# Kernel tuning notes

Measured on AMD Instinct MI355X. Metric: run time of the kernel, lower is better.

## Reference

```python
import jax, jax.numpy as jnp
import numpy as np

STEP, LEAK = 16, 32
KS = STEP + LEAK          # kernel_size = 48
FODEP = KS                # forced depression window
SYNAPSES, NEURONS = 64, 256
IC, OC = 1, 10
DENSE = 0.5
THETA = DENSE * SYNAPSES * IC   # 32.0
BIAS = 0.5
BATCH, TIME = 16, 512


def setup_inputs() -> dict:
    key = jax.random.key(0)
    k1, k2 = jax.random.split(key)
    # binary input spikes, density 0.2
    input_spikes = (jax.random.uniform(k1, (BATCH, IC, SYNAPSES, TIME)) < 0.2).astype(jnp.float32)
    # weight ~ Exponential(rate=1/w_init=2).sample().clip(0,1), mean 0.5
    u = jax.random.uniform(k2, (OC * NEURONS, IC * SYNAPSES), minval=1e-6, maxval=1.0)
    weight = jnp.clip(-0.5 * jnp.log(u), 0.0, 1.0)
    return {"input_spikes": input_spikes, "weight": weight}


def _step_fire_leak_kernel(weight):
    # kernel[o, i, t] = max(0, min(t/step, -(t - w*step)/leak + w)), flipped on t
    t = jnp.arange(KS, dtype=weight.dtype)
    t_spike = t / STEP                                        # rising edge
    t_leak = -(t - weight[..., None] * STEP) / LEAK + weight[..., None]  # decaying edge
    kernel = jnp.maximum(jnp.zeros((), weight.dtype), jnp.minimum(t_spike, t_leak))
    return kernel[..., ::-1]


def _forward(input_spikes, weight):
    B, C, S, T = input_spikes.shape
    x = input_spikes.reshape(B, C * S, T)
    kernel = _step_fire_leak_kernel(weight)                   # [OC*N, IC*S, KS]
    # conv1d with padding = kernel_size on both sides -> T' = T + KS + 1
    pot = jax.lax.conv_general_dilated(
        x, kernel, window_strides=(1,), padding=[(KS, KS)],
        dimension_numbers=("NCH", "OIH", "NCH"))
    Tp = pot.shape[-1]
    pot = pot.reshape(B, OC, NEURONS, Tp) + BIAS * THETA      # unsupervised bias path

    # winner-takes-all scan over time with per-(batch, neuron) depression counter
    pot_t = pot.transpose(3, 0, 2, 1)                         # [T', B, N, OC]
    dep0 = jnp.zeros((B, NEURONS, OC), jnp.int32)

    def step_fn(dep, p):
        masked = jnp.where(dep == 0, p, jnp.zeros((), p.dtype))
        winner = jnp.argmax(masked, axis=-1)                  # [B, N]
        wpot = jnp.take_along_axis(masked, winner[..., None], axis=-1)[..., 0]
        spike = (wpot > THETA).astype(p.dtype)                # [B, N]
        w_t = jax.nn.one_hot(winner, OC, dtype=p.dtype) * spike[..., None]
        dep = jnp.clip(dep + spike.astype(jnp.int32)[..., None] * FODEP - 1, 0, FODEP - 1)
        return dep, w_t

    _, winners = jax.lax.scan(step_fn, dep0, pot_t)           # [T', B, N, OC]
    return winners.transpose(1, 3, 2, 0)                      # [B, OC, N, T'] float


def reference(input_spikes, weight):
    return _forward(input_spikes, weight)
```

## Files before the change

kernel.cpp:

```cpp
#include <hip/hip_runtime.h>

#define B_   16
#define OC_  10
#define N_   256
#define O_   2560
#define S_   64
#define T_   512
#define KS_  48
#define TP_  561
#define TT   24
#define WROW 72

#define NOC   160
#define XROWS 624
#define JC    6
#define NPH   (KS_/JC)

#define SCH    16
#define CPITCH 572

using i32x4 = __attribute__((ext_vector_type(4))) int;

__global__ void prep_all(const float* __restrict__ x, const float* __restrict__ w,
                         unsigned char* __restrict__ xb, signed char* __restrict__ Bg) {
    if (blockIdx.x < 2048) {
        int idx = blockIdx.x * 256 + threadIdx.x;
        int t = idx & 511;
        int bi = idx >> 9;
        int i = bi & 63, b = bi >> 6;
        xb[((size_t)(b * 512 + t) << 6) + i] = (x[idx] != 0.0f) ? 1 : 0;
    } else {
        int idx = (blockIdx.x - 2048) * 256 + threadIdx.x;
        int i = idx & 63;
        int oj = idx >> 6;
        int j = oj % KS_, o = oj / KS_;
        float wv = w[(o << 6) + i];
        float rise = (float)j * 0.0625f;
        float leak = -((float)j - wv * 16.0f) * 0.03125f + wv;
        float kv   = fmaxf(0.0f, fminf(rise, leak));
        int q  = (int)lrintf(kv * 4194304.0f);
        int d0 = ((q + 128) & 255) - 128;
        int q1 = (q - d0) >> 8;
        int d1 = ((q1 + 128) & 255) - 128;
        int d2 = (q1 - d1) >> 8;
        int oc = o >> 4, ol = o & 15;
        int jm = j & 15, jh = j >> 4;
        int pos = jm * 3 + jh;
        int key = (ol >> 1) & 3;
        int bpos = ((((i >> 4) ^ key) << 4) | (i & 15));
        size_t base = (((size_t)(oc * KS_ + pos) * 48) + ol) * 64 + bpos;
        Bg[base]            = (signed char)d0;
        Bg[base + 16 * 64]  = (signed char)d1;
        Bg[base + 32 * 64]  = (signed char)d2;
    }
}

__global__ __launch_bounds__(256, 2) void gemm_i8(
    const unsigned char* __restrict__ xb,
    const signed char*  __restrict__ Bg,
    float* __restrict__ pot)
{
    __shared__ __align__(16) unsigned char xT[XROWS * 64];
    __shared__ __align__(16) signed char  Bst[2][JC * 48 * 64];

    const int tid  = threadIdx.x;
    const int lane = tid & 63;
    const int wave = tid >> 6;
    const int oc = blockIdx.x;
    const int b  = blockIdx.y;
    const int lrow = lane & 15;
    const int quad = lane >> 4;
    const int tw = wave * 144;
    const int coffB = ((quad ^ ((lrow >> 1) & 3)) << 4);

    const signed char* BgBase = Bg + (size_t)oc * KS_ * 48 * 64;

    auto stage = [&](int ph, int buf) {
        const signed char* src = BgBase + (size_t)(ph * JC) * 48 * 64;
        signed char* dst = &Bst[buf][0];
        for (int c = tid; c < JC * 48 * 64 / 16; c += 256)
            __builtin_amdgcn_global_load_lds(
                (const __attribute__((address_space(1))) void*)(src + c * 16),
                (__attribute__((address_space(3))) void*)(dst + c * 16),
                16, 0, 0);
    };

    stage(0, 0);

    for (int z = tid; z < 112 * 4; z += 256) {
        int zi = z >> 2, p = z & 3;
        int r = (zi < 49) ? zi : (561 + zi - 49);
        *(i32x4*)(xT + r * 64 + p * 16) = (i32x4){0, 0, 0, 0};
    }
    const unsigned char* xbb = xb + ((size_t)b << 15);
    for (int q = tid; q < 2048; q += 256) {
        i32x4 v = *(const i32x4*)(xbb + q * 16);
        int t = q >> 2, p = q & 3;
        int r = 49 + t;
        *(i32x4*)(xT + r * 64 + ((p ^ ((r >> 1) & 3)) << 4)) = v;
    }

    i32x4 acc[9][3];
#pragma unroll
    for (int mi = 0; mi < 9; ++mi)
#pragma unroll
        for (int f = 0; f < 3; ++f)
            acc[mi][f] = (i32x4){0, 0, 0, 0};

    __syncthreads();

    for (int ph = 0; ph < NPH; ++ph) {
        if (ph + 1 < NPH) stage(ph + 1, (ph + 1) & 1);
        const signed char* cb = &Bst[ph & 1][0];
#pragma unroll
        for (int tloc = 0; tloc < 2; ++tloc) {
            const int j0 = ph * 2 + tloc;
            const int rb = tw + 16 - j0 + lrow;
            const int coffA = ((quad ^ ((rb >> 1) & 3)) << 4);
            i32x4 af[11], bf[3][3];
#pragma unroll
            for (int k = 0; k < 11; ++k)
                af[k] = *(const i32x4*)(xT + (rb + k * 16) * 64 + coffA);
#pragma unroll
            for (int jh = 0; jh < 3; ++jh)
#pragma unroll
                for (int f = 0; f < 3; ++f)
                    bf[jh][f] = *(const i32x4*)
                        (cb + (((tloc * 3 + jh) * 48) + f * 16 + lrow) * 64 + coffB);
            __builtin_amdgcn_s_setprio(1);
#pragma unroll
            for (int jh = 0; jh < 3; ++jh)
#pragma unroll
                for (int mi = 0; mi < 9; ++mi)
#pragma unroll
                    for (int f = 0; f < 3; ++f)
                        acc[mi][f] = __builtin_amdgcn_mfma_i32_16x16x64_i8(
                            af[mi + 2 - jh], bf[jh][f], acc[mi][f], 0, 0, 0);
            __builtin_amdgcn_s_setprio(0);
        }
        __syncthreads();
    }

    const size_t potb = (size_t)b * TP_;
#pragma unroll
    for (int mi = 0; mi < 9; ++mi) {
#pragma unroll
        for (int r = 0; r < 4; ++r) {
            int t = tw + mi * 16 + quad * 4 + r;
            if (t < TP_) {
                double pq = ((double)acc[mi][0][r]
                           + 256.0   * (double)acc[mi][1][r]
                           + 65536.0 * (double)acc[mi][2][r])
                          * (1.0 / 4194304.0);
                pot[(potb + t) * O_ + oc * 16 + lrow] = (float)pq;
            }
        }
    }
}

__global__ __launch_bounds__(1024) void scan_fused(
    const float* __restrict__ pot,
    float* __restrict__ out)
{
    __shared__ unsigned char codeW[SCH * CPITCH];
    __shared__ unsigned char ocW[SCH * CPITCH];

    const int tid = threadIdx.x;
    const int nc = blockIdx.x;
    const int b  = blockIdx.y;
    const int n0 = nc * SCH;

    for (int pair = tid; pair < TP_ * SCH; pair += 1024) {
        int t = pair >> 4, nl = pair & 15;
        const float* p = pot + ((size_t)(b * TP_ + t)) * O_ + n0 + nl;
        float best = p[0]; int bo = 0;
#pragma unroll
        for (int ch = 1; ch < OC_; ++ch) {
            float v = p[ch * N_];
            if (v > best) { best = v; bo = ch; }
        }
        codeW[nl * CPITCH + t] =
            ((best + 16.0f) > 32.0f) ? (unsigned char)(bo + 1) : (unsigned char)0;
        ocW[nl * CPITCH + t] = 0;
    }
    __syncthreads();

    if (tid < SCH) {
        const unsigned char* c = &codeW[tid * CPITCH];
        unsigned char* o = &ocW[tid * CPITCH];
        int t = 0;
        while (t < TP_) {
            unsigned char buf[KS_];
#pragma unroll
            for (int k = 0; k < KS_; ++k) {
                int tt = t + k;
                buf[k] = (tt < TP_) ? c[tt] : (unsigned char)0;
            }
            int adv = KS_;
#pragma unroll
            for (int k = 0; k < KS_; ++k) {
                if (buf[k]) { o[t + k] = buf[k]; adv = k + KS_; break; }
            }
            t += adv;
        }
    }
    __syncthreads();

    float* ob = out + (((size_t)b * OC_) * N_ + n0) * TP_;
    for (int idx = tid; idx < OC_ * SCH * TP_; idx += 1024) {
        int r = idx / TP_;
        int t = idx - r * TP_;
        int ch = r >> 4, nl = r & 15;
        float v = (ocW[nl * CPITCH + t] == (unsigned char)(ch + 1)) ? 1.0f : 0.0f;
        ob[((size_t)ch * N_ + nl) * TP_ + t] = v;
    }
}

__global__ void transpose_w(const float* __restrict__ w, float* __restrict__ wT) {
    int idx = blockIdx.x * 256 + threadIdx.x;
    if (idx >= O_ * S_) return;
    int o = idx >> 6, i = idx & 63;
    wT[i * O_ + o] = w[idx];
}

__global__ __launch_bounds__(256) void conv_kernel(
    const float* __restrict__ x, const float* __restrict__ wT,
    float* __restrict__ pot)
{
    const int b  = blockIdx.y;
    const int t0 = blockIdx.z * TT;
    const int o  = blockIdx.x * 256 + threadIdx.x;

    __shared__ __align__(16) float xsh[S_][WROW];
    for (int idx = threadIdx.x; idx < S_ * WROW; idx += 256) {
        int i = idx / WROW, m = idx - i * WROW;
        int t = t0 - KS_ + m;
        float v = 0.0f;
        if (t >= 0 && t < T_) v = x[(b * S_ + i) * T_ + t];
        xsh[i][m] = v;
    }
    __syncthreads();

    float acch[TT], accl[TT];
#pragma unroll
    for (int tl = 0; tl < TT; ++tl) { acch[tl] = 0.0f; accl[tl] = 0.0f; }

    for (int i = 0; i < S_; ++i) {
        float xw[WROW];
#pragma unroll
        for (int w4 = 0; w4 < WROW / 4; ++w4) {
            const float4 v = *reinterpret_cast<const float4*>(&xsh[i][w4 * 4]);
            xw[w4 * 4 + 0] = v.x; xw[w4 * 4 + 1] = v.y;
            xw[w4 * 4 + 2] = v.z; xw[w4 * 4 + 3] = v.w;
        }
        const float wv = wT[i * O_ + o];
#pragma unroll
        for (int j = 1; j < KS_; ++j) {
            float rise = (float)j * 0.0625f;
            float leak = -((float)j - wv * 16.0f) * 0.03125f + wv;
            float kv   = fmaxf(0.0f, fminf(rise, leak));
            float khi  = rintf(kv * 4096.0f) * 2.44140625e-4f;
            float klo  = kv - khi;
#pragma unroll
            for (int tl = 0; tl < TT; ++tl) {
                float xv = xw[tl + (KS_ - 1) - j];
                acch[tl] = fmaf(xv, khi, acch[tl]);
                accl[tl] = fmaf(xv, klo, accl[tl]);
            }
        }
    }
#pragma unroll
    for (int tl = 0; tl < TT; ++tl) {
        int t = t0 + tl;
        if (t < TP_) pot[((size_t)b * TP_ + t) * O_ + o] = acch[tl] + accl[tl];
    }
}

__global__ void scan_prep(const float* __restrict__ pot, unsigned char* __restrict__ code) {
    int idx = blockIdx.x * 256 + threadIdx.x;
    if (idx >= B_ * TP_ * N_) return;
    int n  = idx & (N_ - 1);
    int bt = idx >> 8;
    const float* p = pot + (size_t)bt * O_ + n;
    float best = p[0]; int bo = 0;
#pragma unroll
    for (int oc = 1; oc < OC_; ++oc) {
        float v = p[oc * N_];
        if (v > best) { best = v; bo = oc; }
    }
    code[idx] = ((best + 16.0f) > 32.0f) ? (unsigned char)(bo + 1) : (unsigned char)0;
}

__global__ void scan_run(const unsigned char* __restrict__ code, float* __restrict__ out) {
    int idx = blockIdx.x * 256 + threadIdx.x;
    if (idx >= B_ * N_) return;
    int b = idx >> 8, n = idx & 255;
    const unsigned char* c = code + (size_t)b * TP_ * N_ + n;
    int t = 0;
    while (t < TP_) {
        unsigned char buf[KS_];
#pragma unroll
        for (int k = 0; k < KS_; ++k) {
            int tt = t + k;
            buf[k] = (tt < TP_) ? c[(size_t)tt * N_] : (unsigned char)0;
        }
        int adv = KS_;
#pragma unroll
        for (int k = 0; k < KS_; ++k) {
            if (buf[k]) {
                out[(((size_t)b * OC_ + (buf[k] - 1)) * N_ + n) * TP_ + (t + k)] = 1.0f;
                adv = k + KS_;
                break;
            }
        }
        t += adv;
    }
}

extern "C" void kernel_launch(void* const* d_in, const int* in_sizes, int n_in,
                              void* d_out, int out_size, void* d_ws, size_t ws_size,
                              hipStream_t stream) {
    const float* x = (const float*)d_in[0];
    const float* w = (const float*)d_in[1];
    float* out = (float*)d_out;

    char* ws = (char*)d_ws;
    const size_t szX = (size_t)B_ * T_ * S_;
    const size_t szB = (size_t)NOC * KS_ * 48 * 64;
    const size_t szP = (size_t)B_ * TP_ * O_ * 4;
    const size_t szC = (size_t)B_ * TP_ * N_;
    const size_t need = szX + szB + szP + szC;

    if (ws_size >= need) {
        unsigned char* xb  = (unsigned char*)ws;
        signed char* Bg    = (signed char*)(ws + szX);
        float* pot         = (float*)(ws + szX + szB);

        prep_all<<<2048 + 30720, 256, 0, stream>>>(x, w, xb, Bg);
        gemm_i8<<<dim3(NOC, B_), 256, 0, stream>>>(xb, Bg, pot);
        scan_fused<<<dim3(N_ / SCH, B_), 1024, 0, stream>>>(pot, out);
    } else {
        size_t pot_bytes  = (size_t)B_ * TP_ * O_ * sizeof(float);
        size_t code_bytes = (size_t)B_ * TP_ * N_;
        float* pot = (float*)ws;
        unsigned char* code = (unsigned char*)(ws + pot_bytes);
        float* wT = (float*)(ws + pot_bytes + code_bytes);

        hipMemsetAsync(d_out, 0, (size_t)out_size * sizeof(float), stream);
        transpose_w<<<(O_ * S_ + 255) / 256, 256, 0, stream>>>(w, wT);
        conv_kernel<<<dim3(O_ / 256, B_, (TP_ + TT - 1) / TT), 256, 0, stream>>>(x, wT, pot);
        scan_prep<<<(B_ * TP_ * N_ + 255) / 256, 256, 0, stream>>>(pot, code);
        scan_run<<<(B_ * N_ + 255) / 256, 256, 0, stream>>>(code, out);
    }
}
```

Baseline: 272.2 us.

## Load weight fragments directly from global into registers, drop LDS staging

Removes the double-buffered LDS staging of the B (weight) tiles via global_load_lds and the per-phase block barriers. Each lane now loads its B fragments straight from global memory into registers, register double-buffered across time-offset steps, and the prep kernel drops the XOR swizzle from the B layout. This frees LDS and avoids barriers, but puts global load latency directly in the MFMA loop and raises register pressure.

```diff
diff --git a/kernel.cpp b/kernel.cpp
--- a/kernel.cpp
+++ b/kernel.cpp
@@ -13,8 +13,6 @@
 
 #define NOC   160
 #define XROWS 624
-#define JC    6
-#define NPH   (KS_/JC)
 
 #define SCH    16
 #define CPITCH 572
@@ -46,9 +44,7 @@
         int oc = o >> 4, ol = o & 15;
         int jm = j & 15, jh = j >> 4;
         int pos = jm * 3 + jh;
-        int key = (ol >> 1) & 3;
-        int bpos = ((((i >> 4) ^ key) << 4) | (i & 15));
-        size_t base = (((size_t)(oc * KS_ + pos) * 48) + ol) * 64 + bpos;
+        size_t base = (((size_t)(oc * KS_ + pos) * 48) + ol) * 64 + i;
         Bg[base]            = (signed char)d0;
         Bg[base + 16 * 64]  = (signed char)d1;
         Bg[base + 32 * 64]  = (signed char)d2;
@@ -61,7 +57,6 @@
     float* __restrict__ pot)
 {
     __shared__ __align__(16) unsigned char xT[XROWS * 64];
-    __shared__ __align__(16) signed char  Bst[2][JC * 48 * 64];
 
     const int tid  = threadIdx.x;
     const int lane = tid & 63;
@@ -71,21 +66,9 @@
     const int lrow = lane & 15;
     const int quad = lane >> 4;
     const int tw = wave * 144;
-    const int coffB = ((quad ^ ((lrow >> 1) & 3)) << 4);
-
-    const signed char* BgBase = Bg + (size_t)oc * KS_ * 48 * 64;
-
-    auto stage = [&](int ph, int buf) {
-        const signed char* src = BgBase + (size_t)(ph * JC) * 48 * 64;
-        signed char* dst = &Bst[buf][0];
-        for (int c = tid; c < JC * 48 * 64 / 16; c += 256)
-            __builtin_amdgcn_global_load_lds(
-                (const __attribute__((address_space(1))) void*)(src + c * 16),
-                (__attribute__((address_space(3))) void*)(dst + c * 16),
-                16, 0, 0);
-    };
-
-    stage(0, 0);
+
+    const signed char* Bgb = Bg + (size_t)oc * (KS_ * 48 * 64)
+                           + lrow * 64 + quad * 16;
 
     for (int z = tid; z < 112 * 4; z += 256) {
         int zi = z >> 2, p = z & 3;
@@ -107,38 +90,43 @@
         for (int f = 0; f < 3; ++f)
             acc[mi][f] = (i32x4){0, 0, 0, 0};
 
+    i32x4 bfA[9], bfB[9];
+
+    auto loadB = [&](int t, i32x4 (&d)[9]) {
+#pragma unroll
+        for (int jh = 0; jh < 3; ++jh)
+#pragma unroll
+            for (int f = 0; f < 3; ++f)
+                d[jh * 3 + f] = *(const i32x4*)(Bgb + (t * 3 + jh) * 3072 + f * 1024);
+    };
+
+    auto tlocBody = [&](int t, const i32x4 (&bf)[9]) {
+        const int rb = tw + 16 - t + lrow;
+        const int coffA = ((quad ^ ((rb >> 1) & 3)) << 4);
+        i32x4 af[11];
+#pragma unroll
+        for (int k = 0; k < 11; ++k)
+            af[k] = *(const i32x4*)(xT + (rb + k * 16) * 64 + coffA);
+        __builtin_amdgcn_s_setprio(1);
+#pragma unroll
+        for (int jh = 0; jh < 3; ++jh)
+#pragma unroll
+            for (int mi = 0; mi < 9; ++mi)
+#pragma unroll
+                for (int f = 0; f < 3; ++f)
+                    acc[mi][f] = __builtin_amdgcn_mfma_i32_16x16x64_i8(
+                        af[mi + 2 - jh], bf[jh * 3 + f], acc[mi][f], 0, 0, 0);
+        __builtin_amdgcn_s_setprio(0);
+    };
+
     __syncthreads();
 
-    for (int ph = 0; ph < NPH; ++ph) {
-        if (ph + 1 < NPH) stage(ph + 1, (ph + 1) & 1);
-        const signed char* cb = &Bst[ph & 1][0];
-#pragma unroll
-        for (int tloc = 0; tloc < 2; ++tloc) {
-            const int j0 = ph * 2 + tloc;
-            const int rb = tw + 16 - j0 + lrow;
-            const int coffA = ((quad ^ ((rb >> 1) & 3)) << 4);
-            i32x4 af[11], bf[3][3];
-#pragma unroll
-            for (int k = 0; k < 11; ++k)
-                af[k] = *(const i32x4*)(xT + (rb + k * 16) * 64 + coffA);
-#pragma unroll
-            for (int jh = 0; jh < 3; ++jh)
-#pragma unroll
-                for (int f = 0; f < 3; ++f)
-                    bf[jh][f] = *(const i32x4*)
-                        (cb + (((tloc * 3 + jh) * 48) + f * 16 + lrow) * 64 + coffB);
-            __builtin_amdgcn_s_setprio(1);
-#pragma unroll
-            for (int jh = 0; jh < 3; ++jh)
-#pragma unroll
-                for (int mi = 0; mi < 9; ++mi)
-#pragma unroll
-                    for (int f = 0; f < 3; ++f)
-                        acc[mi][f] = __builtin_amdgcn_mfma_i32_16x16x64_i8(
-                            af[mi + 2 - jh], bf[jh][f], acc[mi][f], 0, 0, 0);
-            __builtin_amdgcn_s_setprio(0);
-        }
-        __syncthreads();
+    loadB(0, bfA);
+    for (int tp = 0; tp < 8; ++tp) {
+        loadB(2 * tp + 1, bfB);
+        tlocBody(2 * tp, bfA);
+        if (tp < 7) loadB(2 * tp + 2, bfA);
+        tlocBody(2 * tp + 1, bfB);
     }
 
     const size_t potb = (size_t)b * TP_;
```

Result: faster. 258.4 us (-5.1%).
